# Kernel optimization log

Measured on AMD Instinct MI355X. Metric: run time of the kernel, lower is better.

The kernel has to match this reference:

```python
import jax, jax.numpy as jnp
from jax import lax
import numpy as np

MD = 3            # max displacement -> 7x7 = 49 correlation channels
DBL_BACKWARD = 2.5  # dblBackward[intLevel=4]
NEG_SLOPE = 0.1


def lrelu(x):
    return jnp.where(x >= 0, x, NEG_SLOPE * x)


def conv2d(x, w, b, pad):
    y = lax.conv_general_dilated(x, w, (1, 1), [(pad, pad), (pad, pad)],
                                 dimension_numbers=('NCHW', 'OIHW', 'NCHW'))
    return y + b[None, :, None, None]


def upflow(flow, wu):
    # torch ConvTranspose2d(2,2,k=4,s=2,p=1,groups=2,bias=False) == conv with
    # lhs_dilation=2, padding=k-1-p=2, flipped kernel, feature_group_count=2
    wf = jnp.flip(wu, (-2, -1))  # [2,1,4,4]
    return lax.conv_general_dilated(flow, wf, (1, 1), [(2, 2), (2, 2)],
                                    lhs_dilation=(2, 2),
                                    dimension_numbers=('NCHW', 'OIHW', 'NCHW'),
                                    feature_group_count=2)


def bilinear_zeros(img, x, y):
    # img [B,C,H,W]; x,y [B,H,W] pixel coords (align_corners=True semantics),
    # zeros padding outside.
    B, C, H, W = img.shape
    x0 = jnp.floor(x); y0 = jnp.floor(y)
    x1 = x0 + 1.0;     y1 = y0 + 1.0
    wa = (x1 - x) * (y1 - y); wb = (x - x0) * (y1 - y)
    wc = (x1 - x) * (y - y0); wd = (x - x0) * (y - y0)
    bidx = jnp.arange(B)[:, None, None]

    def gather(yi, xi):
        valid = (xi >= 0) & (xi <= W - 1) & (yi >= 0) & (yi <= H - 1)
        xc = jnp.clip(xi, 0, W - 1).astype(jnp.int32)
        yc = jnp.clip(yi, 0, H - 1).astype(jnp.int32)
        v = img[bidx, :, yc, xc]  # [B,H,W,C]
        return v * valid[..., None].astype(img.dtype)

    out = (gather(y0, x0) * wa[..., None] + gather(y0, x1) * wb[..., None] +
           gather(y1, x0) * wc[..., None] + gather(y1, x1) * wd[..., None])
    return jnp.transpose(out, (0, 3, 1, 2))


def backward_warp(inp, flow):
    # LiteFlowNet Backward(): warp + occlusion mask from warped ones-channel
    B, C, H, W = inp.shape
    gy, gx = jnp.meshgrid(jnp.arange(H, dtype=inp.dtype),
                          jnp.arange(W, dtype=inp.dtype), indexing='ij')
    x = gx[None] + flow[:, 0]
    y = gy[None] + flow[:, 1]
    img1 = jnp.concatenate([inp, jnp.ones((B, 1, H, W), inp.dtype)], axis=1)
    out = bilinear_zeros(img1, x, y)
    mask = (out[:, -1:] > 0.999).astype(inp.dtype)
    return out[:, :-1] * mask


def correlation(first, second):
    # 7x7 local cost volume, stride 1, normalized by channel count
    B, C, H, W = first.shape
    pad = jnp.pad(second, ((0, 0), (0, 0), (MD, MD), (MD, MD)))
    slabs = []
    for dy in range(2 * MD + 1):
        for dx in range(2 * MD + 1):
            shifted = lax.dynamic_slice(pad, (0, 0, dy, dx), (B, C, H, W))
            slabs.append(jnp.mean(first * shifted, axis=1))  # [B,H,W]
    return jnp.stack(slabs, axis=1)  # [B,49,H,W]


def setup_inputs() -> dict:
    key = jax.random.key(0)
    ks = jax.random.split(key, 16)
    B, C, H, W = 16, 96, 128, 128
    inp = {
        'tensorFirst':  jax.random.normal(ks[0], (B, 3, 256, 256), jnp.float32),
        'tensorSecond': jax.random.normal(ks[1], (B, 3, 256, 256), jnp.float32),
        'tensorFeaturesFirst':  jax.random.normal(ks[2], (B, C, H, W), jnp.float32),
        'tensorFeaturesSecond': jax.random.normal(ks[3], (B, C, H, W), jnp.float32),
        'tensorFlow': jax.random.normal(ks[4], (B, 2, H // 2, W // 2), jnp.float32),
        'wu': jax.random.normal(ks[5], (2, 1, 4, 4), jnp.float32) * 0.25,
        'w1': jax.random.normal(ks[6], (128, 49, 3, 3), jnp.float32) * 0.05,
        'b1': jnp.zeros((128,), jnp.float32),
        'w2': jax.random.normal(ks[7], (64, 128, 3, 3), jnp.float32) * 0.05,
        'b2': jnp.zeros((64,), jnp.float32),
        'w3': jax.random.normal(ks[8], (32, 64, 3, 3), jnp.float32) * 0.05,
        'b3': jnp.zeros((32,), jnp.float32),
        'w4': jax.random.normal(ks[9], (2, 32, 5, 5), jnp.float32) * 0.05,
        'b4': jnp.zeros((2,), jnp.float32),
    }
    return inp


def reference(tensorFirst, tensorSecond, tensorFeaturesFirst, tensorFeaturesSecond,
              tensorFlow, wu, w1, b1, w2, b2, w3, b3, w4, b4):
    # intLevel=4: moduleFeat is identity
    flow = upflow(tensorFlow, wu)                                  # [B,2,128,128]
    feat2 = backward_warp(tensorFeaturesSecond, flow * DBL_BACKWARD)
    corr = lrelu(correlation(tensorFeaturesFirst, feat2))          # [B,49,H,W]
    x = lrelu(conv2d(corr, w1, b1, 1))
    x = lrelu(conv2d(x, w2, b2, 1))
    x = lrelu(conv2d(x, w3, b3, 1))
    x = conv2d(x, w4, b4, 2)
    return flow + x
```

## Files before the change

### kernel.cpp

```cpp
#include <hip/hip_runtime.h>

typedef unsigned short u16;
typedef unsigned int u32;
typedef short short8 __attribute__((ext_vector_type(8)));
typedef float f32x4 __attribute__((ext_vector_type(4)));

#define HW 128

__device__ __forceinline__ float bf2f(u16 h) {
    u32 u = ((u32)h) << 16;
    return __uint_as_float(u);
}
__device__ __forceinline__ u16 f2bf(float f) {
    u32 u = __float_as_uint(f);
    u32 r = (u + 0x7FFFu + ((u >> 16) & 1u)) >> 16;
    return (u16)r;
}
__device__ __forceinline__ float lrelu_f(float v) {
    return v >= 0.f ? v : 0.1f * v;
}

__device__ __forceinline__ void gload_lds16(const void* g, void* l) {
    __builtin_amdgcn_global_load_lds((const __attribute__((address_space(1))) void*)g,
                                     (__attribute__((address_space(3))) void*)l, 16, 0, 0);
}

template<int ICR, int ICP, int OC>
__global__ __launch_bounds__(256) void pack_w(const float* __restrict__ w, u16* __restrict__ dst) {
    constexpr int NCH = ICP / 32;
    constexpr int NTOT = 9 * NCH * 4 * OC * 8;
    int gid = blockIdx.x * 256 + threadIdx.x;
    if (gid >= NTOT) return;
    int j = gid & 7;
    int t = gid >> 3;
    int oc = t % OC; t /= OC;
    int quad = t & 3; t >>= 2;
    int ch = t % NCH;
    int tap = t / NCH;
    int ic = ch * 32 + quad * 8 + j;
    int ky = tap / 3, kx = tap % 3;
    float v = (ic < ICR) ? w[((oc * ICR + ic) * 3 + ky) * 3 + kx] : 0.f;
    dst[gid] = f2bf(v);
}

__global__ __launch_bounds__(256) void pack_w4(const float* __restrict__ w, float* __restrict__ dst) {
    int gid = blockIdx.x * 256 + threadIdx.x;
    if (gid >= 1600) return;
    int ic = gid & 31;
    int t = gid >> 5;
    int oc = t & 1;
    int tap = t >> 1;
    dst[(tap * 2 + oc) * 32 + ic] = w[(oc * 32 + ic) * 25 + tap];
}

__global__ __launch_bounds__(256) void upflow_kernel(const float* __restrict__ tflow, const float* __restrict__ wu,
                                                     float* __restrict__ flow) {
    int gid = blockIdx.x * 256 + threadIdx.x;
    int x = gid & 127;
    int y = (gid >> 7) & 127;
    int c = (gid >> 14) & 1;
    int b = gid >> 15;
    float acc = 0.f;
#pragma unroll
    for (int ky = 0; ky < 4; ++ky) {
        int u = y + ky - 2;
        if ((u & 1) || u < 0 || u > 126) continue;
        int iy = u >> 1;
#pragma unroll
        for (int kx = 0; kx < 4; ++kx) {
            int v = x + kx - 2;
            if ((v & 1) || v < 0 || v > 126) continue;
            int ix = v >> 1;
            acc += tflow[((b * 2 + c) * 64 + iy) * 64 + ix] *
                   wu[c * 16 + (3 - ky) * 4 + (3 - kx)];
        }
    }
    flow[gid] = acc;
}

__global__ __launch_bounds__(256) void warp_kernel(const float* __restrict__ second, const float* __restrict__ flow,
                                                   u16* __restrict__ feat2) {
    int tid = threadIdx.x;
    int x = tid & 127;
    int half = tid >> 7;
    int blk = blockIdx.x;
    int cgp = blk % 6;
    int t = blk / 6;
    int y = t & 127;
    int b = t >> 7;
    int cg = cgp * 2 + half;

    float fx = (float)x + 2.5f * flow[((b * 2 + 0) * HW + y) * HW + x];
    float fy = (float)y + 2.5f * flow[((b * 2 + 1) * HW + y) * HW + x];
    float x0f = floorf(fx), y0f = floorf(fy);
    int x0 = (int)x0f, y0 = (int)y0f;
    int x1 = x0 + 1, y1 = y0 + 1;
    float wx1 = fx - x0f, wx0 = (x0f + 1.f) - fx;
    float wy1 = fy - y0f, wy0 = (y0f + 1.f) - fy;
    float wA = wx0 * wy0, wB = wx1 * wy0, wC = wx0 * wy1, wD = wx1 * wy1;
    float vA = (x0 >= 0 && x0 <= 127 && y0 >= 0 && y0 <= 127) ? 1.f : 0.f;
    float vB = (x1 >= 0 && x1 <= 127 && y0 >= 0 && y0 <= 127) ? 1.f : 0.f;
    float vC = (x0 >= 0 && x0 <= 127 && y1 >= 0 && y1 <= 127) ? 1.f : 0.f;
    float vD = (x1 >= 0 && x1 <= 127 && y1 >= 0 && y1 <= 127) ? 1.f : 0.f;
    wA *= vA; wB *= vB; wC *= vC; wD *= vD;
    float ones = wA + wB + wC + wD;
    float maskf = (ones > 0.999f) ? 1.f : 0.f;
    wA *= maskf; wB *= maskf; wC *= maskf; wD *= maskf;
    int xc0 = min(max(x0, 0), 127), xc1 = min(max(x1, 0), 127);
    int yc0 = min(max(y0, 0), 127), yc1 = min(max(y1, 0), 127);
    int i00 = yc0 * HW + xc0, i01 = yc0 * HW + xc1;
    int i10 = yc1 * HW + xc0, i11 = yc1 * HW + xc1;

    const float* base = second + (size_t)b * 96 * HW * HW + (size_t)(cg * 8) * (HW * HW);
    short8 o;
#pragma unroll
    for (int j = 0; j < 8; ++j) {
        const float* pp = base + (size_t)j * (HW * HW);
        float v = wA * pp[i00] + wB * pp[i01] + wC * pp[i10] + wD * pp[i11];
        o[j] = (short)f2bf(v);
    }
    *(short8*)(feat2 + ((((size_t)(b * 134) + y + 3) * 12 + cg) * 144 + (x + 3)) * 8) = o;
}

__global__ __launch_bounds__(256) void corr_mfma(const float* __restrict__ first, const u16* __restrict__ feat2,
                                                 u16* __restrict__ corrp) {
    int tid = threadIdx.x;
    int wave = tid >> 6, lane = tid & 63;
    int quad = lane >> 4, l16 = lane & 15;
    int blk = blockIdx.x;
    int half = blk & 1;
    int y = (blk >> 1) & 127;
    int b = blk >> 8;
    int x0 = (half * 4 + wave) * 16;

    short8 afr[3];
    const float* fbase = first + ((size_t)(b * 96) * HW + y) * HW + x0 + l16;
#pragma unroll
    for (int ch = 0; ch < 3; ++ch) {
        short8 a;
#pragma unroll
        for (int j = 0; j < 8; ++j)
            a[j] = (short)f2bf(fbase[(size_t)(ch * 32 + quad * 8 + j) * (HW * HW)]);
        afr[ch] = a;
    }

    f32x4 acc[7][2];
#pragma unroll
    for (int dy = 0; dy < 7; ++dy) {
        acc[dy][0] = (f32x4){0.f, 0.f, 0.f, 0.f};
        acc[dy][1] = (f32x4){0.f, 0.f, 0.f, 0.f};
    }

#pragma unroll
    for (int dy = 0; dy < 7; ++dy) {
#pragma unroll
        for (int ch = 0; ch < 3; ++ch) {
            const u16* rp = feat2 + ((((size_t)(b * 134) + y + dy) * 12 + ch * 4 + quad) * 144 + x0 + l16) * 8;
            short8 b0 = *(const short8*)(rp);
            short8 b1 = *(const short8*)(rp + 16 * 8);
            acc[dy][0] = __builtin_amdgcn_mfma_f32_16x16x32_bf16(afr[ch], b0, acc[dy][0], 0, 0, 0);
            acc[dy][1] = __builtin_amdgcn_mfma_f32_16x16x32_bf16(afr[ch], b1, acc[dy][1], 0, 0, 0);
        }
    }

    u16* op = corrp + ((size_t)(b * 130) + y + 1) * (130 * 64);
#pragma unroll
    for (int dy = 0; dy < 7; ++dy)
#pragma unroll
        for (int nt = 0; nt < 2; ++nt)
#pragma unroll
            for (int r = 0; r < 4; ++r) {
                int m = quad * 4 + r;
                int dx = nt * 16 + l16 - m;
                if (dx >= 0 && dx < 7) {
                    float v = lrelu_f(acc[dy][nt][r] * (1.f / 96.f));
                    op[(size_t)(x0 + m + 1) * 64 + dy * 7 + dx] = f2bf(v);
                }
            }
}

template<int ICP, int OC, int OCB, int PADOUT>
__global__ __launch_bounds__(256, 4) void conv_mfma(const u16* __restrict__ in, const u16* __restrict__ wp,
                                                    const float* __restrict__ bias, u16* __restrict__ out) {
    constexpr int NCH = ICP / 32;
    constexpr int NOCT = OCB / 16;
    constexpr int OCG = OC / OCB;
    constexpr int Wi = 130;
    constexpr int Wo = 128 + 2 * PADOUT;

    __shared__ __align__(16) u16 ldsA[4 * 144 * 32];

    int tid = threadIdx.x;
    int wave = tid >> 6, lane = tid & 63;
    int quad = lane >> 4, l16 = lane & 15;

    int cpx = gridDim.x >> 3;
    int bid = blockIdx.x;
    int swz = (bid & 7) * cpx + (bid >> 3);
    int rowpair = swz & 63;
    int t = swz >> 6;
    int ocg = t % OCG;
    int b = t / OCG;
    int row_blk = rowpair * 2;
    int row_h = wave >> 1;
    int px0 = (wave & 1) * 64;

    f32x4 acc[4][NOCT];
#pragma unroll
    for (int mt = 0; mt < 4; ++mt)
#pragma unroll
        for (int ot = 0; ot < NOCT; ++ot)
            acc[mt][ot] = (f32x4){0.f, 0.f, 0.f, 0.f};

    int pxl = lane >> 2;
    int g   = lane & 3;

    for (int s = 0; s < NCH; ++s) {
        {
            const u16* rbase = in + ((size_t)(b * Wi + row_blk + wave) * Wi) * ICP + s * 32;
            u16* lbase = &ldsA[wave * (144 * 32)];
#pragma unroll
            for (int c = 0; c < 9; ++c) {
                int px = c * 16 + pxl;
                int q = (g ^ (px >> 1)) & 3;
                int pxg = px > 129 ? 129 : px;
                const u16* src = rbase + (size_t)pxg * ICP + q * 8;
                gload_lds16(src, lbase + c * 16 * 32);
            }
        }
        __syncthreads();

#pragma unroll
        for (int ky = 0; ky < 3; ++ky) {
#pragma unroll
            for (int kx = 0; kx < 3; ++kx) {
                const u16* bptr = wp + ((((size_t)(ky * 3 + kx) * NCH + s) * 4 + quad) * OC + ocg * OCB + l16) * 8;
                short8 bfr[NOCT];
#pragma unroll
                for (int ot = 0; ot < NOCT; ++ot)
                    bfr[ot] = *(const short8*)(bptr + ot * 16 * 8);
                short8 afr[4];
#pragma unroll
                for (int mt = 0; mt < 4; ++mt) {
                    int rpx = px0 + kx + mt * 16 + l16;
                    int gg = (quad ^ (rpx >> 1)) & 3;
                    afr[mt] = *(const short8*)&ldsA[((row_h + ky) * 144 + rpx) * 32 + gg * 8];
                }
#pragma unroll
                for (int mt = 0; mt < 4; ++mt)
#pragma unroll
                    for (int ot = 0; ot < NOCT; ++ot)
                        acc[mt][ot] = __builtin_amdgcn_mfma_f32_16x16x32_bf16(afr[mt], bfr[ot], acc[mt][ot], 0, 0, 0);
            }
        }
        __syncthreads();
    }

    float bv[NOCT];
#pragma unroll
    for (int ot = 0; ot < NOCT; ++ot) bv[ot] = bias[ocg * OCB + ot * 16 + l16];

#pragma unroll
    for (int mt = 0; mt < 4; ++mt) {
#pragma unroll
        for (int ot = 0; ot < NOCT; ++ot) {
#pragma unroll
            for (int r = 0; r < 4; ++r) {
                int px = px0 + mt * 16 + quad * 4 + r;
                float v = lrelu_f(acc[mt][ot][r] + bv[ot]);
                out[((size_t)(b * Wo + row_blk + row_h + PADOUT) * Wo + px + PADOUT) * OC + ocg * OCB + ot * 16 + l16] = f2bf(v);
            }
        }
    }
}

__global__ __launch_bounds__(256) void conv4_kernel(const u16* __restrict__ in, const float* __restrict__ w4p,
                                                    const float* __restrict__ b4, const float* __restrict__ flow,
                                                    float* __restrict__ out) {
    int gid = blockIdx.x * 256 + threadIdx.x;
    int x = gid & 127;
    int y = (gid >> 7) & 127;
    int b = gid >> 14;
    float acc0 = b4[0], acc1 = b4[1];
#pragma unroll
    for (int ky = 0; ky < 5; ++ky) {
#pragma unroll
        for (int kx = 0; kx < 5; ++kx) {
            const u16* p = in + ((size_t)(b * 132 + y + ky) * 132 + x + kx) * 32;
            const float* wb = w4p + (ky * 5 + kx) * 64;
#pragma unroll
            for (int g = 0; g < 4; ++g) {
                short8 vv = *(const short8*)(p + g * 8);
#pragma unroll
                for (int j = 0; j < 8; ++j) {
                    float v = bf2f((u16)vv[j]);
                    acc0 += v * wb[g * 8 + j];
                    acc1 += v * wb[32 + g * 8 + j];
                }
            }
        }
    }
    int o0 = ((b * 2 + 0) * HW + y) * HW + x;
    int o1 = o0 + HW * HW;
    out[o0] = acc0 + flow[o0];
    out[o1] = acc1 + flow[o1];
}

extern "C" void kernel_launch(void* const* d_in, const int* in_sizes, int n_in,
                              void* d_out, int out_size, void* d_ws, size_t ws_size,
                              hipStream_t stream) {
    const float* ffirst  = (const float*)d_in[2];
    const float* fsecond = (const float*)d_in[3];
    const float* tflow   = (const float*)d_in[4];
    const float* wu      = (const float*)d_in[5];
    const float* w1 = (const float*)d_in[6];
    const float* b1 = (const float*)d_in[7];
    const float* w2 = (const float*)d_in[8];
    const float* b2 = (const float*)d_in[9];
    const float* w3 = (const float*)d_in[10];
    const float* b3 = (const float*)d_in[11];
    const float* w4 = (const float*)d_in[12];
    const float* b4 = (const float*)d_in[13];
    float* out = (float*)d_out;
    char* ws = (char*)d_ws;

    u16* w1p = (u16*)(ws + 0);
    u16* w2p = (u16*)(ws + 147456);
    u16* w3p = (u16*)(ws + 294912);
    float* w4p = (float*)(ws + 331776);

    float* flow = (float*)(ws + 602112);
    u16* regA = (u16*)(ws + 2699264);
    u16* regB = (u16*)(ws + 71921664);

    pack_w<49, 64, 128><<<288, 256, 0, stream>>>(w1, w1p);
    pack_w<128, 128, 64><<<288, 256, 0, stream>>>(w2, w2p);
    pack_w<64, 64, 32><<<72, 256, 0, stream>>>(w3, w3p);
    pack_w4<<<7, 256, 0, stream>>>(w4, w4p);

    upflow_kernel<<<2048, 256, 0, stream>>>(tflow, wu, flow);

    hipMemsetAsync(regA, 0, 59277312, stream);
    warp_kernel<<<12288, 256, 0, stream>>>(fsecond, flow, regA);

    hipMemsetAsync(regB, 0, 34611200, stream);
    corr_mfma<<<4096, 256, 0, stream>>>(ffirst, regA, regB);

    hipMemsetAsync(regA, 0, 69222400, stream);
    conv_mfma<64, 128, 64, 1><<<2048, 256, 0, stream>>>(regB, w1p, b1, regA);

    hipMemsetAsync(regB, 0, 34611200, stream);
    conv_mfma<128, 64, 64, 1><<<1024, 256, 0, stream>>>(regA, w2p, b2, regB);

    hipMemsetAsync(regA, 0, 17842176, stream);
    conv_mfma<64, 32, 32, 2><<<1024, 256, 0, stream>>>(regB, w3p, b3, regA);

    conv4_kernel<<<1024, 256, 0, stream>>>(regA, w4p, b4, flow, out);
}
```

Baseline: 625.3 us.

## Replace full-buffer memsets with border-only zeroing and double-buffer conv LDS staging

Full hipMemsetAsync clears of the intermediate activation buffers are replaced by small kernels that zero only the halo/border pixels. The correlation kernel now explicitly zeroes its unused padding channels 49-63. The conv kernel double-buffers its LDS input tile so the next channel chunk's global-to-LDS load overlaps the current chunk's MFMAs, which removes one barrier per iteration. This doubles LDS use and lowers the occupancy hint from 4 to 2 blocks. The main cost targeted is roughly 200MB of memset traffic, with a risk of race or correctness issues, since the loop now has only one sync per chunk.

```diff
diff --git a/kernel.cpp b/kernel.cpp
--- a/kernel.cpp
+++ b/kernel.cpp
@@ -51,6 +51,55 @@
     int oc = t & 1;
     int tap = t >> 1;
     dst[(tap * 2 + oc) * 32 + ic] = w[(oc * 32 + ic) * 25 + tap];
+}
+
+template<int S, int LO, int NI, int C>
+__global__ __launch_bounds__(256) void zero_border(u16* __restrict__ buf) {
+    constexpr int MID = S - NI;
+    constexpr int NB = S * S - NI * NI;
+    constexpr int TOP = LO * S;
+    int idx = blockIdx.x * 256 + threadIdx.x;
+    if (idx >= 16 * NB) return;
+    int b = idx / NB;
+    int r = idx - b * NB;
+    int y, x;
+    if (r < TOP) { y = r / S; x = r - y * S; }
+    else if (r < TOP + NI * MID) {
+        int rr = r - TOP;
+        y = LO + rr / MID;
+        int c0 = rr - (rr / MID) * MID;
+        x = c0 < LO ? c0 : c0 + NI;
+    } else {
+        int rr = r - TOP - NI * MID;
+        y = LO + NI + rr / S;
+        x = rr - (rr / S) * S;
+    }
+    u16* p = buf + ((size_t)(b * S + y) * S + x) * C;
+#pragma unroll
+    for (int c = 0; c < C; c += 8)
+        *(short8*)(p + c) = (short8){0, 0, 0, 0, 0, 0, 0, 0};
+}
+
+__global__ __launch_bounds__(256) void zero_feat2_halo(u16* __restrict__ f) {
+    constexpr int FULLROWS = 6 * 12 * 144;
+    constexpr int PER_B = FULLROWS + 128 * 12 * 16;
+    int idx = blockIdx.x * 256 + threadIdx.x;
+    if (idx >= 16 * PER_B) return;
+    int b = idx / PER_B;
+    int r = idx - b * PER_B;
+    int row, cg, x;
+    if (r < FULLROWS) {
+        x = r % 144; int t = r / 144;
+        cg = t % 12; int k = t / 12;
+        row = k < 3 ? k : 128 + k;
+    } else {
+        int rr = r - FULLROWS;
+        int c0 = rr & 15; int t = rr >> 4;
+        cg = t % 12; row = 3 + t / 12;
+        x = c0 < 3 ? c0 : c0 + 128;
+    }
+    *(short8*)(f + ((((size_t)(b * 134) + row) * 12 + cg) * 144 + x) * 8) =
+        (short8){0, 0, 0, 0, 0, 0, 0, 0};
 }
 
 __global__ __launch_bounds__(256) void upflow_kernel(const float* __restrict__ tflow, const float* __restrict__ wu,
@@ -177,10 +226,18 @@
                     op[(size_t)(x0 + m + 1) * 64 + dy * 7 + dx] = f2bf(v);
                 }
             }
+
+    if (l16 < 15) {
+#pragma unroll
+        for (int r = 0; r < 4; ++r) {
+            int m = quad * 4 + r;
+            op[(size_t)(x0 + m + 1) * 64 + 49 + l16] = 0;
+        }
+    }
 }
 
 template<int ICP, int OC, int OCB, int PADOUT>
-__global__ __launch_bounds__(256, 4) void conv_mfma(const u16* __restrict__ in, const u16* __restrict__ wp,
+__global__ __launch_bounds__(256, 2) void conv_mfma(const u16* __restrict__ in, const u16* __restrict__ wp,
                                                     const float* __restrict__ bias, u16* __restrict__ out) {
     constexpr int NCH = ICP / 32;
     constexpr int NOCT = OCB / 16;
@@ -188,7 +245,7 @@
     constexpr int Wi = 130;
     constexpr int Wo = 128 + 2 * PADOUT;
 
-    __shared__ __align__(16) u16 ldsA[4 * 144 * 32];
+    __shared__ __align__(16) u16 ldsA[2][4 * 144 * 32];
 
     int tid = threadIdx.x;
     int wave = tid >> 6, lane = tid & 63;
@@ -205,6 +262,21 @@
     int row_h = wave >> 1;
     int px0 = (wave & 1) * 64;
 
+    int pxl = lane >> 2;
+    int g   = lane & 3;
+
+    auto stageA = [&](int s) {
+        const u16* rbase = in + ((size_t)(b * Wi + row_blk + wave) * Wi) * ICP + s * 32;
+        u16* lbase = &ldsA[s & 1][wave * (144 * 32)];
+#pragma unroll
+        for (int c = 0; c < 9; ++c) {
+            int px = c * 16 + pxl;
+            int q = (g ^ (px >> 1)) & 3;
+            int pxg = px > 129 ? 129 : px;
+            gload_lds16(rbase + (size_t)pxg * ICP + q * 8, lbase + c * 16 * 32);
+        }
+    };
+
     f32x4 acc[4][NOCT];
 #pragma unroll
     for (int mt = 0; mt < 4; ++mt)
@@ -212,24 +284,12 @@
         for (int ot = 0; ot < NOCT; ++ot)
             acc[mt][ot] = (f32x4){0.f, 0.f, 0.f, 0.f};
 
-    int pxl = lane >> 2;
-    int g   = lane & 3;
+    stageA(0);
+    __syncthreads();
 
     for (int s = 0; s < NCH; ++s) {
-        {
-            const u16* rbase = in + ((size_t)(b * Wi + row_blk + wave) * Wi) * ICP + s * 32;
-            u16* lbase = &ldsA[wave * (144 * 32)];
-#pragma unroll
-            for (int c = 0; c < 9; ++c) {
-                int px = c * 16 + pxl;
-                int q = (g ^ (px >> 1)) & 3;
-                int pxg = px > 129 ? 129 : px;
-                const u16* src = rbase + (size_t)pxg * ICP + q * 8;
-                gload_lds16(src, lbase + c * 16 * 32);
-            }
-        }
-        __syncthreads();
-
+        if (s + 1 < NCH) stageA(s + 1);
+        const u16* lA = &ldsA[s & 1][0];
 #pragma unroll
         for (int ky = 0; ky < 3; ++ky) {
 #pragma unroll
@@ -244,7 +304,7 @@
                 for (int mt = 0; mt < 4; ++mt) {
                     int rpx = px0 + kx + mt * 16 + l16;
                     int gg = (quad ^ (rpx >> 1)) & 3;
-                    afr[mt] = *(const short8*)&ldsA[((row_h + ky) * 144 + rpx) * 32 + gg * 8];
+                    afr[mt] = *(const short8*)&lA[((row_h + ky) * 144 + rpx) * 32 + gg * 8];
                 }
 #pragma unroll
                 for (int mt = 0; mt < 4; ++mt)
@@ -340,19 +400,19 @@
 
     upflow_kernel<<<2048, 256, 0, stream>>>(tflow, wu, flow);
 
-    hipMemsetAsync(regA, 0, 59277312, stream);
+    zero_feat2_halo<<<2184, 256, 0, stream>>>(regA);
     warp_kernel<<<12288, 256, 0, stream>>>(fsecond, flow, regA);
 
-    hipMemsetAsync(regB, 0, 34611200, stream);
+    zero_border<130, 1, 128, 64><<<33, 256, 0, stream>>>(regB);
     corr_mfma<<<4096, 256, 0, stream>>>(ffirst, regA, regB);
 
-    hipMemsetAsync(regA, 0, 69222400, stream);
+    zero_border<130, 1, 128, 128><<<33, 256, 0, stream>>>(regA);
     conv_mfma<64, 128, 64, 1><<<2048, 256, 0, stream>>>(regB, w1p, b1, regA);
 
-    hipMemsetAsync(regB, 0, 34611200, stream);
+    zero_border<130, 1, 128, 64><<<33, 256, 0, stream>>>(regB);
     conv_mfma<128, 64, 64, 1><<<1024, 256, 0, stream>>>(regA, w2p, b2, regB);
 
-    hipMemsetAsync(regA, 0, 17842176, stream);
+    zero_border<132, 2, 128, 32><<<65, 256, 0, stream>>>(regA);
     conv_mfma<64, 32, 32, 2><<<1024, 256, 0, stream>>>(regB, w3p, b3, regA);
 
     conv4_kernel<<<1024, 256, 0, stream>>>(regA, w4p, b4, flow, out);
```

Measured after the change: 558.5 us. 10.7% less time.
